# Performance work log

Hardware: AMD Instinct MI355X
Metric: run time of the kernel (lower is better)

The kernel has to match this reference:

```python
import jax, jax.numpy as jnp
import numpy as np

D_MODEL = 1024
N_BLOCK = 20
EPS = 1e-8


def setup_inputs() -> dict:
    key = jax.random.key(0)
    k = jax.random.split(key, 7)
    B, S, D, NB = 8, 2048, D_MODEL, N_BLOCK
    e = jax.random.normal(k[0], (B, S, D), dtype=jnp.float32)
    m = jax.random.normal(k[1], (B, S, D), dtype=jnp.float32)
    state = jax.random.normal(k[2], (1, NB * D), dtype=jnp.float32)
    # learned params of the EntNet-style RNN_cell
    U = jax.random.normal(k[3], (D, D), dtype=jnp.float32) * 0.02
    V = jax.random.normal(k[4], (D, D), dtype=jnp.float32) * 0.02
    W = jax.random.normal(k[5], (D, D), dtype=jnp.float32) * 0.02
    keys = jax.random.normal(k[6], (NB, D), dtype=jnp.float32) * 0.02
    return {"e": e, "m": m, "state": state, "U": U, "V": V, "W": W, "keys": keys}


def reference(e, m, state, U, V, W, keys):
    B, S, D = e.shape
    NB = keys.shape[0]
    h0 = state.reshape(NB, D)  # shared initial memory state across batch
    x = e + m  # combined per-timestep input, (B, S, D)

    def step(h, xt):  # h: (NB, D), xt: (D,)
        # per-slot gate: content similarity + key similarity
        g = jax.nn.sigmoid(h @ xt + keys @ xt)  # (NB,)
        # candidate memory
        cand = jnp.tanh(h @ U.T + keys @ V.T + (W @ xt)[None, :])  # (NB, D)
        h = h + g[:, None] * cand
        # per-slot L2 normalization
        h = h / (jnp.linalg.norm(h, axis=1, keepdims=True) + EPS)
        return h, None

    def run(xseq):  # xseq: (S, D) -> final state (NB, D)
        hT, _ = jax.lax.scan(step, h0, xseq)
        return hT

    out = jax.vmap(run)(x)  # (B, NB, D)
    return out
```

## Files before the change

### kernel.cpp

```cpp
#include <hip/hip_runtime.h>
#include <cstdint>
#include <cstddef>

namespace {

constexpr int D   = 1024;
constexpr int NB  = 20;
constexpr int B   = 8;
constexpr int S   = 2048;
constexpr int NWG = 32;
constexpr float EPS = 1e-8f;

typedef __attribute__((ext_vector_type(4))) float f4_t;
typedef __attribute__((ext_vector_type(8))) short s8_t;
typedef unsigned long long u64_t;

__device__ __forceinline__ unsigned short f2bf(float f) {
  unsigned u = __float_as_uint(f);
  u += 0x7fffu + ((u >> 16) & 1u);
  return (unsigned short)(u >> 16);
}
__device__ __forceinline__ float bf2f(unsigned short h) {
  return __uint_as_float(((unsigned)h) << 16);
}
__device__ __forceinline__ float u64lo(u64_t x) { return __uint_as_float((unsigned)x); }
__device__ __forceinline__ float u64hi(u64_t x) { return __uint_as_float((unsigned)(x >> 32)); }
__device__ __forceinline__ float rcp_f(float x) { return __builtin_amdgcn_rcpf(x); }
__device__ __forceinline__ float sigm_fast(float x) { return rcp_f(1.0f + __expf(-x)); }
__device__ __forceinline__ float tanh_fast(float x) {
  const float e = __expf(2.0f * x);
  return 1.0f - 2.0f * rcp_f(e + 1.0f);
}

#define MFMA(a, b, c) __builtin_amdgcn_mfma_f32_16x16x32_bf16((a), (b), (c), 0, 0, 0)
#define ALOAD64(p) __hip_atomic_load((p), __ATOMIC_RELAXED, __HIP_MEMORY_SCOPE_AGENT)
#define ASTORE64(p, v) __hip_atomic_store((p), (v), __ATOMIC_RELAXED, __HIP_MEMORY_SCOPE_AGENT)
#define ALOAD32(p) __hip_atomic_load((p), __ATOMIC_RELAXED, __HIP_MEMORY_SCOPE_AGENT)
#define ASTORE32(p, v) __hip_atomic_store((p), (v), __ATOMIC_RELAXED, __HIP_MEMORY_SCOPE_AGENT)

constexpr size_t OFF_HBUF = 0;
constexpr size_t OFF_NORM = OFF_HBUF + 2ull * B * NB * 512 * 4;
constexpr size_t OFF_CTR  = OFF_NORM + 2ull * B * NB * NWG * 4;
constexpr size_t OFF_KV   = OFF_CTR + (size_t)B * 32 * 4;
constexpr size_t OFF_KX   = OFF_KV + (size_t)NB * D * 4;
constexpr size_t OFF_UHI  = OFF_KX + (size_t)B * S * NB * 4;
constexpr size_t OFF_ULO  = OFF_UHI + (size_t)D * D * 2;
constexpr size_t OFF_WHI  = OFF_ULO + (size_t)D * D * 2;
constexpr size_t OFF_WLO  = OFF_WHI + (size_t)D * D * 2;


__global__ void k_convert(const float* __restrict__ U, const float* __restrict__ W,
                          unsigned short* __restrict__ Uhi, unsigned short* __restrict__ Ulo,
                          unsigned short* __restrict__ Whi, unsigned short* __restrict__ Wlo) {
  const int n = D * D;
  for (int i = blockIdx.x * blockDim.x + threadIdx.x; i < n; i += gridDim.x * blockDim.x) {
    float u = U[i];
    unsigned short h = f2bf(u);
    Uhi[i] = h;
    Ulo[i] = f2bf(u - bf2f(h));
    float w = W[i];
    h = f2bf(w);
    Whi[i] = h;
    Wlo[i] = f2bf(w - bf2f(h));
  }
}

__global__ void k_kv(const float* __restrict__ keys, const float* __restrict__ V,
                     float* __restrict__ KV) {
  const int tid = threadIdx.x;
  const int j = blockIdx.x * 64 + (tid >> 2);
  const int kq = tid & 3;
  const f4_t* v4 = (const f4_t*)(V + (size_t)j * D + kq * 256);
  const f4_t* k4base = (const f4_t*)keys;
  float acc[NB];
#pragma unroll
  for (int i = 0; i < NB; ++i) acc[i] = 0.f;
  for (int q = 0; q < 64; ++q) {
    const f4_t v = v4[q];
#pragma unroll
    for (int i = 0; i < NB; ++i) {
      const f4_t kk = k4base[i * 256 + kq * 64 + q];
      acc[i] += kk[0] * v[0] + kk[1] * v[1] + kk[2] * v[2] + kk[3] * v[3];
    }
  }
#pragma unroll
  for (int i = 0; i < NB; ++i) {
    float s = acc[i];
    s += __shfl_xor(s, 1);
    s += __shfl_xor(s, 2);
    if (kq == 0) KV[(size_t)i * D + j] = s;
  }
}

__global__ void k_kx(const float* __restrict__ e, const float* __restrict__ m,
                     const float* __restrict__ keys, float* __restrict__ KX) {
  __shared__ f4_t xs[256];
  __shared__ float part[NB][8];
  const int bt = blockIdx.x, tid = threadIdx.x;
  xs[tid] = ((const f4_t*)e)[(size_t)bt * 256 + tid] + ((const f4_t*)m)[(size_t)bt * 256 + tid];
  __syncthreads();
  if (tid < 160) {
    const int i = tid >> 3, s8 = tid & 7;
    float acc = 0.f;
    const f4_t* k4 = (const f4_t*)keys + i * 256 + s8 * 32;
    for (int q = 0; q < 32; ++q) {
      const f4_t kk = k4[q];
      const f4_t xx = xs[s8 * 32 + q];
      acc += kk[0] * xx[0] + kk[1] * xx[1] + kk[2] * xx[2] + kk[3] * xx[3];
    }
    part[i][s8] = acc;
  }
  __syncthreads();
  if (tid < NB) {
    float s = 0.f;
#pragma unroll
    for (int q = 0; q < 8; ++q) s += part[tid][q];
    KX[(size_t)bt * NB + tid] = s;
  }
}

__global__ void k_state(const float* __restrict__ state, unsigned* __restrict__ Hbuf,
                        float* __restrict__ NormP, int* __restrict__ ctr) {
  const int idx = blockIdx.x * 256 + threadIdx.x;
  if (idx < B * NB * 512) {
    const int r = idx % (NB * 512);
    const int i = r >> 9, d2 = (r & 511) << 1;
    const unsigned short a = f2bf(state[i * D + d2]);
    const unsigned short c = f2bf(state[i * D + d2 + 1]);
    Hbuf[idx] = (unsigned)a | ((unsigned)c << 16);
  }
  const int j = idx - B * NB * 512;
  if (j >= 0 && j < B * NB * NWG) NormP[j] = 1.0f / 32.0f;
  const int q = idx - B * NB * 512 - B * NB * NWG;
  if (q >= 0 && q < B * 32) ctr[q] = 0;
}


struct __align__(16) LdsT {
  unsigned short hnA[NB * 1024];
  unsigned short xtA[2][1024];
  float credU[4][2][2][16][20];
  float wxAcc[4][2][16];
  float gAcc[4][2][16];
  float KVs[NB][32];
  float ownH[NB][32];
  float pad_force_1_block_per_cu[3072];
};

__device__ __forceinline__ void build_xt(unsigned short* xt , int tid, f4_t x) {
  const unsigned short h0 = f2bf(x[0]), h1 = f2bf(x[1]), h2 = f2bf(x[2]), h3 = f2bf(x[3]);
  const unsigned short u0 = f2bf(x[0] - bf2f(h0)), u1 = f2bf(x[1] - bf2f(h1));
  const unsigned short u2 = f2bf(x[2] - bf2f(h2)), u3 = f2bf(x[3] - bf2f(h3));
  const int kp = tid << 2;
  *(unsigned*)&xt[kp] = (unsigned)h0 | ((unsigned)h1 << 16);
  *(unsigned*)&xt[kp + 2] = (unsigned)h2 | ((unsigned)h3 << 16);
  *(unsigned*)&xt[1024 + kp] = (unsigned)u0 | ((unsigned)u1 << 16);
  *(unsigned*)&xt[1024 + kp + 2] = (unsigned)u2 | ((unsigned)u3 << 16);
}

__device__ __forceinline__ void stage_h(unsigned short* hn, int tid, const u64_t* hv) {
  const int blkk = tid >> 1;
  const int half = (tid & 1) << 2;
#pragma unroll
  for (int j = 0; j < 20; ++j)
    *(u64_t*)&hn[(j << 10) + ((blkk ^ (j & 15)) << 3) + half] = hv[j];
}

__device__ __forceinline__ void bar_lds() {
  asm volatile("s_waitcnt lgkmcnt(0)\n\ts_barrier" ::: "memory");
}
__device__ __forceinline__ void bar_full() {
  asm volatile("s_waitcnt vmcnt(0) lgkmcnt(0)\n\ts_barrier" ::: "memory");
}

__device__ __forceinline__ void poll32(const unsigned* fb, int ln31, int wg,
                                       unsigned tgt, unsigned pv) {
  if (__ballot(pv >= tgt) == ~0ull) return;
  for (;;) {
    const unsigned v = (ln31 == wg) ? tgt : ALOAD32(fb + ln31);
    if (__ballot(v >= tgt) == ~0ull) return;
    __builtin_amdgcn_s_sleep(1);
  }
}

__launch_bounds__(256, 1)
__global__ void k_rnn(const float* __restrict__ e, const float* __restrict__ m,
                      const float* __restrict__ state,
                      const float* __restrict__ KX, const float* __restrict__ KV,
                      const unsigned short* __restrict__ Uhi, const unsigned short* __restrict__ Ulo,
                      const unsigned short* __restrict__ Whi, const unsigned short* __restrict__ Wlo,
                      unsigned* __restrict__ Hbuf, float* __restrict__ NormP,
                      int* __restrict__ ctr, float* __restrict__ out) {
  __shared__ LdsT L;
  const int tid = threadIdx.x;
  const int b = blockIdx.x >> 5;
  const int wg = blockIdx.x & 31;
  const int wv = tid >> 6;
  const int ln = tid & 63;
  const int l15 = ln & 15;
  const int lo4 = ln >> 4;
  const int ln31 = tid & 31;
  unsigned* ctrp = (unsigned*)ctr + b * 32;

  s8_t BUh[2][8], BUl[2][8], BWh[2][8], BWl[2][8];
  {
    const int rowb = (wg << 5) + l15;
#pragma unroll
    for (int nt = 0; nt < 2; ++nt)
#pragma unroll
      for (int kf = 0; kf < 8; ++kf) {
        const size_t off = (size_t)(rowb + nt * 16) * D + (wv << 8) + (kf << 5) + (lo4 << 3);
        BUh[nt][kf] = *(const s8_t*)(Uhi + off);
        BUl[nt][kf] = *(const s8_t*)(Ulo + off);
        BWh[nt][kf] = *(const s8_t*)(Whi + off);
        BWl[nt][kf] = *(const s8_t*)(Wlo + off);
      }
  }
  if (tid < 160) {
    const int i = tid >> 3, c4 = (tid & 7) << 2;
    *(f4_t*)&L.ownH[i][c4] = *(const f4_t*)(state + (size_t)i * D + (wg << 5) + c4);
    *(f4_t*)&L.KVs[i][c4] = *(const f4_t*)(KV + (size_t)i * D + (wg << 5) + c4);
  }

  f4_t evv, mvv;
  float sreg = 1.f;
  float kxreg = 0.f;

  {
    u64_t hv[20];
    const u64_t* hb8 = (const u64_t*)Hbuf + (size_t)(0 * B + b) * (NB * 256);
#pragma unroll
    for (int j = 0; j < 20; ++j) hv[j] = ALOAD64(hb8 + j * 256 + tid);
    const f4_t x0 = ((const f4_t*)e)[(size_t)(b * S) * 256 + tid] +
                    ((const f4_t*)m)[(size_t)(b * S) * 256 + tid];
    build_xt(&L.xtA[0][0], tid, x0);
    stage_h(L.hnA, tid, hv);
    if (tid < 160) kxreg = KX[(size_t)(b * S) * NB + (tid >> 3)];
    evv = ((const f4_t*)e)[(size_t)(b * S + 1) * 256 + tid];
    mvv = ((const f4_t*)m)[(size_t)(b * S + 1) * 256 + tid];
  }
  __syncthreads();

  for (int t = 0; t < S; ++t) {
    const int nxt2 = (t + 1) & 1;

    f4_t cU00 = {0, 0, 0, 0}, cU01 = {0, 0, 0, 0}, cU10 = {0, 0, 0, 0}, cU11 = {0, 0, 0, 0};
    f4_t cW0 = {0, 0, 0, 0}, cW1 = {0, 0, 0, 0}, cG0 = {0, 0, 0, 0}, cG1 = {0, 0, 0, 0};
    {
      const unsigned short* hb = L.hnA;
      const unsigned short* xb = &L.xtA[0][0];
      const int r1 = 16 + (l15 < 4 ? l15 : 3);
#pragma unroll
      for (int kf = 0; kf < 8; ++kf) {
        const int blk = (wv << 5) + (kf << 2) + lo4;
        const s8_t a0 = *(const s8_t*)&hb[(l15 << 10) + ((blk ^ l15) << 3)];
        const s8_t a1 = *(const s8_t*)&hb[(r1 << 10) + ((blk ^ (r1 & 15)) << 3)];
        const s8_t ax = *(const s8_t*)&xb[(l15 & 1) * 1024 + (blk << 3)];
        cU00 = MFMA(a0, BUh[0][kf], cU00);
        cU00 = MFMA(a0, BUl[0][kf], cU00);
        cU01 = MFMA(a0, BUh[1][kf], cU01);
        cU01 = MFMA(a0, BUl[1][kf], cU01);
        cU10 = MFMA(a1, BUh[0][kf], cU10);
        cU10 = MFMA(a1, BUl[0][kf], cU10);
        cU11 = MFMA(a1, BUh[1][kf], cU11);
        cU11 = MFMA(a1, BUl[1][kf], cU11);
        cW0 = MFMA(ax, BWh[0][kf], cW0);
        cW0 = MFMA(ax, BWl[0][kf], cW0);
        cW1 = MFMA(ax, BWh[1][kf], cW1);
        cW1 = MFMA(ax, BWl[1][kf], cW1);
        cG0 = MFMA(ax, a0, cG0);
        cG1 = MFMA(ax, a1, cG1);
      }
    }
#pragma unroll
    for (int q = 0; q < 4; ++q) {
      const int r = (lo4 << 2) + q;
      L.credU[wv][0][0][r][l15] = cU00[q];
      L.credU[wv][0][1][r][l15] = cU01[q];
      L.credU[wv][1][0][r][l15] = cU10[q];
      L.credU[wv][1][1][r][l15] = cU11[q];
    }
    if (lo4 == 0) {
      L.wxAcc[wv][0][l15] = cW0[0] + cW0[1];
      L.wxAcc[wv][1][l15] = cW1[0] + cW1[1];
      L.gAcc[wv][0][l15] = cG0[0] + cG0[1];
      L.gAcc[wv][1][l15] = cG1[0] + cG1[1];
    }
    bar_lds();

    unsigned pv = 0;
    if (t + 1 < S) pv = (ln31 == wg) ? (unsigned)(t + 1) : ALOAD32(ctrp + ln31);

    if (tid < 160) {
      const int i = tid >> 3, c4 = (tid & 7) << 2;
      const int mt = i >> 4, r = i & 15, nt = c4 >> 4, ccc = c4 & 15;
      const f4_t sU = *(const f4_t*)&L.credU[0][mt][nt][r][ccc] +
                      *(const f4_t*)&L.credU[1][mt][nt][r][ccc] +
                      *(const f4_t*)&L.credU[2][mt][nt][r][ccc] +
                      *(const f4_t*)&L.credU[3][mt][nt][r][ccc];
      const f4_t wx = *(const f4_t*)&L.wxAcc[0][nt][ccc] +
                      *(const f4_t*)&L.wxAcc[1][nt][ccc] +
                      *(const f4_t*)&L.wxAcc[2][nt][ccc] +
                      *(const f4_t*)&L.wxAcc[3][nt][ccc];
      const f4_t kv = *(const f4_t*)&L.KVs[i][c4];
      const f4_t oh = *(const f4_t*)&L.ownH[i][c4];
      const float s = sreg;
      const float gpre = s * (L.gAcc[0][mt][r] + L.gAcc[1][mt][r] +
                              L.gAcc[2][mt][r] + L.gAcc[3][mt][r]) + kxreg;
      const float g = sigm_fast(gpre);
      f4_t hn;
      float sq = 0.f;
#pragma unroll
      for (int u = 0; u < 4; ++u) {
        const float cand = tanh_fast(s * sU[u] + kv[u] + wx[u]);
        const float hx = s * oh[u] + g * cand;
        hn[u] = hx;
        sq += hx * hx;
      }
      *(f4_t*)&L.ownH[i][c4] = hn;
      const unsigned d0 = (unsigned)f2bf(hn[0]) | ((unsigned)f2bf(hn[1]) << 16);
      const unsigned d1 = (unsigned)f2bf(hn[2]) | ((unsigned)f2bf(hn[3]) << 16);
      u64_t* hb8 = (u64_t*)Hbuf + (size_t)(nxt2 * B + b) * (NB * 256) +
                   (i << 8) + (wg << 3) + (c4 >> 2);
      ASTORE64(hb8, (u64_t)d0 | ((u64_t)d1 << 32));
      sq += __shfl_xor(sq, 1);
      sq += __shfl_xor(sq, 2);
      sq += __shfl_xor(sq, 4);
      if ((tid & 7) == 0) {
        unsigned* np = (unsigned*)NormP + ((size_t)(nxt2 * B + b) * NB + i) * NWG + wg;
        ASTORE32(np, __float_as_uint(sq));
      }
    }
    bar_full();

    if (tid == 0) ASTORE32(ctrp + wg, (unsigned)(t + 1));

    if (t + 1 < S) {
      poll32(ctrp, ln31, wg, (unsigned)(t + 1), pv);
      u64_t hv[20];
      const u64_t* g0 = (const u64_t*)Hbuf + (size_t)(nxt2 * B + b) * (NB * 256);
#pragma unroll
      for (int j = 0; j < 20; ++j) hv[j] = ALOAD64(g0 + j * 256 + tid);
      float np0 = 0.f;
      if (tid < 160) {
        const int i = tid >> 3;
        const u64_t* n0 = (const u64_t*)NormP + ((size_t)(nxt2 * B + b) * NB + i) * 16 + ((tid & 7) << 1);
        const u64_t a0 = ALOAD64(n0);
        const u64_t a1 = ALOAD64(n0 + 1);
        np0 = u64lo(a0) + u64hi(a0) + u64lo(a1) + u64hi(a1);
        kxreg = KX[((size_t)b * S + t + 1) * NB + i];
      }
      build_xt(&L.xtA[0][0], tid, evv + mvv);
      if (t + 2 < S) {
        evv = ((const f4_t*)e)[(size_t)(b * S + t + 2) * 256 + tid];
        mvv = ((const f4_t*)m)[(size_t)(b * S + t + 2) * 256 + tid];
      }
      stage_h(L.hnA, tid, hv);
      if (tid < 160) {
        float s0 = np0;
        s0 += __shfl_xor(s0, 1);
        s0 += __shfl_xor(s0, 2);
        s0 += __shfl_xor(s0, 4);
        sreg = rcp_f(sqrtf(s0) + EPS);
      }
    }
    bar_lds();
  }

  poll32(ctrp, ln31, wg, (unsigned)S, 0u);
  if (tid < 160) {
    const int i = tid >> 3, c4 = (tid & 7) << 2;
    const u64_t* np8 = (const u64_t*)NormP + ((size_t)(0 * B + b) * NB + i) * 16 + ((tid & 7) << 1);
    const u64_t x0 = ALOAD64(np8);
    const u64_t x1 = ALOAD64(np8 + 1);
    float sq = u64lo(x0) + u64hi(x0) + u64lo(x1) + u64hi(x1);
    sq += __shfl_xor(sq, 1);
    sq += __shfl_xor(sq, 2);
    sq += __shfl_xor(sq, 4);
    const float sc = rcp_f(sqrtf(sq) + EPS);
    const f4_t oh = *(const f4_t*)&L.ownH[i][c4];
    f4_t ov;
#pragma unroll
    for (int u = 0; u < 4; ++u) ov[u] = sc * oh[u];
    *(f4_t*)(out + (size_t)b * NB * D + (size_t)i * D + (wg << 5) + c4) = ov;
  }
}

}

extern "C" void kernel_launch(void* const* d_in, const int* in_sizes, int n_in,
                              void* d_out, int out_size, void* d_ws, size_t ws_size,
                              hipStream_t stream) {
  const float* e = (const float*)d_in[0];
  const float* m = (const float*)d_in[1];
  const float* state = (const float*)d_in[2];
  const float* U = (const float*)d_in[3];
  const float* V = (const float*)d_in[4];
  const float* W = (const float*)d_in[5];
  const float* keys = (const float*)d_in[6];
  float* out = (float*)d_out;
  char* ws = (char*)d_ws;

  unsigned* Hbuf = (unsigned*)(ws + OFF_HBUF);
  float* NormP = (float*)(ws + OFF_NORM);
  int* ctr = (int*)(ws + OFF_CTR);
  float* KV = (float*)(ws + OFF_KV);
  float* KX = (float*)(ws + OFF_KX);
  unsigned short* Uhi = (unsigned short*)(ws + OFF_UHI);
  unsigned short* Ulo = (unsigned short*)(ws + OFF_ULO);
  unsigned short* Whi = (unsigned short*)(ws + OFF_WHI);
  unsigned short* Wlo = (unsigned short*)(ws + OFF_WLO);

  k_convert<<<512, 256, 0, stream>>>(U, W, Uhi, Ulo, Whi, Wlo);
  k_kv<<<16, 256, 0, stream>>>(keys, V, KV);
  k_kx<<<B * S, 256, 0, stream>>>(e, m, keys, KX);
  k_state<<<342, 256, 0, stream>>>(state, Hbuf, NormP, ctr);
  k_rnn<<<B * NWG, 256, 0, stream>>>(e, m, state, KX, KV, Uhi, Ulo, Whi, Wlo,
                                     Hbuf, NormP, ctr, out);
}
```

Before: 11.89 ms.

## Double workgroup size to 512 threads splitting K across 8 waves

```diff
diff --git a/kernel.cpp b/kernel.cpp
--- a/kernel.cpp
+++ b/kernel.cpp
@@ -11,6 +11,7 @@
 constexpr int NWG = 32;
 constexpr float EPS = 1e-8f;
 
+typedef __attribute__((ext_vector_type(2))) float f2_t;
 typedef __attribute__((ext_vector_type(4))) float f4_t;
 typedef __attribute__((ext_vector_type(8))) short s8_t;
 typedef unsigned long long u64_t;
@@ -139,31 +140,30 @@
 struct __align__(16) LdsT {
   unsigned short hnA[NB * 1024];
   unsigned short xtA[2][1024];
-  float credU[4][2][2][16][20];
-  float wxAcc[4][2][16];
-  float gAcc[4][2][16];
+  float credU[8][2][2][16][20];
+  float wxAcc[8][2][16];
+  float gAcc[8][2][16];
   float KVs[NB][32];
   float ownH[NB][32];
-  float pad_force_1_block_per_cu[3072];
 };
 
-__device__ __forceinline__ void build_xt(unsigned short* xt , int tid, f4_t x) {
-  const unsigned short h0 = f2bf(x[0]), h1 = f2bf(x[1]), h2 = f2bf(x[2]), h3 = f2bf(x[3]);
+__device__ __forceinline__ void build_xt(unsigned short* xt , int tid, f2_t x) {
+  const unsigned short h0 = f2bf(x[0]), h1 = f2bf(x[1]);
   const unsigned short u0 = f2bf(x[0] - bf2f(h0)), u1 = f2bf(x[1] - bf2f(h1));
-  const unsigned short u2 = f2bf(x[2] - bf2f(h2)), u3 = f2bf(x[3] - bf2f(h3));
-  const int kp = tid << 2;
+  const int kp = tid << 1;
   *(unsigned*)&xt[kp] = (unsigned)h0 | ((unsigned)h1 << 16);
-  *(unsigned*)&xt[kp + 2] = (unsigned)h2 | ((unsigned)h3 << 16);
   *(unsigned*)&xt[1024 + kp] = (unsigned)u0 | ((unsigned)u1 << 16);
-  *(unsigned*)&xt[1024 + kp + 2] = (unsigned)u2 | ((unsigned)u3 << 16);
-}
-
-__device__ __forceinline__ void stage_h(unsigned short* hn, int tid, const u64_t* hv) {
-  const int blkk = tid >> 1;
-  const int half = (tid & 1) << 2;
-#pragma unroll
-  for (int j = 0; j < 20; ++j)
-    *(u64_t*)&hn[(j << 10) + ((blkk ^ (j & 15)) << 3) + half] = hv[j];
+}
+
+__device__ __forceinline__ void stage_h(unsigned short* hn, int t8, int rbase,
+                                        const u64_t* hv) {
+  const int blkk = t8 >> 1;
+  const int halfo = (t8 & 1) << 2;
+#pragma unroll
+  for (int j = 0; j < 10; ++j) {
+    const int jr = rbase + j;
+    *(u64_t*)&hn[(jr << 10) + ((blkk ^ (jr & 15)) << 3) + halfo] = hv[j];
+  }
 }
 
 __device__ __forceinline__ void bar_lds() {
@@ -183,7 +183,7 @@
   }
 }
 
-__launch_bounds__(256, 1)
+__launch_bounds__(512, 2)
 __global__ void k_rnn(const float* __restrict__ e, const float* __restrict__ m,
                       const float* __restrict__ state,
                       const float* __restrict__ KX, const float* __restrict__ KV,
@@ -193,23 +193,25 @@
                       int* __restrict__ ctr, float* __restrict__ out) {
   __shared__ LdsT L;
   const int tid = threadIdx.x;
-  const int b = blockIdx.x >> 5;
-  const int wg = blockIdx.x & 31;
+  const int b = blockIdx.x & 7;
+  const int wg = blockIdx.x >> 3;
   const int wv = tid >> 6;
   const int ln = tid & 63;
   const int l15 = ln & 15;
   const int lo4 = ln >> 4;
   const int ln31 = tid & 31;
+  const int t8 = tid & 255;
+  const int rbase = (tid >> 8) * 10;
   unsigned* ctrp = (unsigned*)ctr + b * 32;
 
-  s8_t BUh[2][8], BUl[2][8], BWh[2][8], BWl[2][8];
+  s8_t BUh[2][4], BUl[2][4], BWh[2][4], BWl[2][4];
   {
     const int rowb = (wg << 5) + l15;
 #pragma unroll
     for (int nt = 0; nt < 2; ++nt)
 #pragma unroll
-      for (int kf = 0; kf < 8; ++kf) {
-        const size_t off = (size_t)(rowb + nt * 16) * D + (wv << 8) + (kf << 5) + (lo4 << 3);
+      for (int kf = 0; kf < 4; ++kf) {
+        const size_t off = (size_t)(rowb + nt * 16) * D + (wv << 7) + (kf << 5) + (lo4 << 3);
         BUh[nt][kf] = *(const s8_t*)(Uhi + off);
         BUl[nt][kf] = *(const s8_t*)(Ulo + off);
         BWh[nt][kf] = *(const s8_t*)(Whi + off);
@@ -222,22 +224,22 @@
     *(f4_t*)&L.KVs[i][c4] = *(const f4_t*)(KV + (size_t)i * D + (wg << 5) + c4);
   }
 
-  f4_t evv, mvv;
+  f2_t evv, mvv;
   float sreg = 1.f;
   float kxreg = 0.f;
 
   {
-    u64_t hv[20];
+    u64_t hv[10];
     const u64_t* hb8 = (const u64_t*)Hbuf + (size_t)(0 * B + b) * (NB * 256);
 #pragma unroll
-    for (int j = 0; j < 20; ++j) hv[j] = ALOAD64(hb8 + j * 256 + tid);
-    const f4_t x0 = ((const f4_t*)e)[(size_t)(b * S) * 256 + tid] +
-                    ((const f4_t*)m)[(size_t)(b * S) * 256 + tid];
+    for (int j = 0; j < 10; ++j) hv[j] = ALOAD64(hb8 + (rbase + j) * 256 + t8);
+    const f2_t x0 = ((const f2_t*)e)[(size_t)(b * S) * 512 + tid] +
+                    ((const f2_t*)m)[(size_t)(b * S) * 512 + tid];
     build_xt(&L.xtA[0][0], tid, x0);
-    stage_h(L.hnA, tid, hv);
+    stage_h(L.hnA, t8, rbase, hv);
     if (tid < 160) kxreg = KX[(size_t)(b * S) * NB + (tid >> 3)];
-    evv = ((const f4_t*)e)[(size_t)(b * S + 1) * 256 + tid];
-    mvv = ((const f4_t*)m)[(size_t)(b * S + 1) * 256 + tid];
+    evv = ((const f2_t*)e)[(size_t)(b * S + 1) * 512 + tid];
+    mvv = ((const f2_t*)m)[(size_t)(b * S + 1) * 512 + tid];
   }
   __syncthreads();
 
@@ -251,8 +253,8 @@
       const unsigned short* xb = &L.xtA[0][0];
       const int r1 = 16 + (l15 < 4 ? l15 : 3);
 #pragma unroll
-      for (int kf = 0; kf < 8; ++kf) {
-        const int blk = (wv << 5) + (kf << 2) + lo4;
+      for (int kf = 0; kf < 4; ++kf) {
+        const int blk = (wv << 4) + (kf << 2) + lo4;
         const s8_t a0 = *(const s8_t*)&hb[(l15 << 10) + ((blk ^ l15) << 3)];
         const s8_t a1 = *(const s8_t*)&hb[(r1 << 10) + ((blk ^ (r1 & 15)) << 3)];
         const s8_t ax = *(const s8_t*)&xb[(l15 & 1) * 1024 + (blk << 3)];
@@ -294,20 +296,18 @@
     if (tid < 160) {
       const int i = tid >> 3, c4 = (tid & 7) << 2;
       const int mt = i >> 4, r = i & 15, nt = c4 >> 4, ccc = c4 & 15;
-      const f4_t sU = *(const f4_t*)&L.credU[0][mt][nt][r][ccc] +
-                      *(const f4_t*)&L.credU[1][mt][nt][r][ccc] +
-                      *(const f4_t*)&L.credU[2][mt][nt][r][ccc] +
-                      *(const f4_t*)&L.credU[3][mt][nt][r][ccc];
-      const f4_t wx = *(const f4_t*)&L.wxAcc[0][nt][ccc] +
-                      *(const f4_t*)&L.wxAcc[1][nt][ccc] +
-                      *(const f4_t*)&L.wxAcc[2][nt][ccc] +
-                      *(const f4_t*)&L.wxAcc[3][nt][ccc];
+      f4_t sU = {0, 0, 0, 0}, wx = {0, 0, 0, 0};
+      float gp = 0.f;
+#pragma unroll
+      for (int w = 0; w < 8; ++w) {
+        sU += *(const f4_t*)&L.credU[w][mt][nt][r][ccc];
+        wx += *(const f4_t*)&L.wxAcc[w][nt][ccc];
+        gp += L.gAcc[w][mt][r];
+      }
       const f4_t kv = *(const f4_t*)&L.KVs[i][c4];
       const f4_t oh = *(const f4_t*)&L.ownH[i][c4];
       const float s = sreg;
-      const float gpre = s * (L.gAcc[0][mt][r] + L.gAcc[1][mt][r] +
-                              L.gAcc[2][mt][r] + L.gAcc[3][mt][r]) + kxreg;
-      const float g = sigm_fast(gpre);
+      const float g = sigm_fast(s * gp + kxreg);
       f4_t hn;
       float sq = 0.f;
 #pragma unroll
@@ -337,10 +337,10 @@
 
     if (t + 1 < S) {
       poll32(ctrp, ln31, wg, (unsigned)(t + 1), pv);
-      u64_t hv[20];
+      u64_t hv[10];
       const u64_t* g0 = (const u64_t*)Hbuf + (size_t)(nxt2 * B + b) * (NB * 256);
 #pragma unroll
-      for (int j = 0; j < 20; ++j) hv[j] = ALOAD64(g0 + j * 256 + tid);
+      for (int j = 0; j < 10; ++j) hv[j] = ALOAD64(g0 + (rbase + j) * 256 + t8);
       float np0 = 0.f;
       if (tid < 160) {
         const int i = tid >> 3;
@@ -352,10 +352,10 @@
       }
       build_xt(&L.xtA[0][0], tid, evv + mvv);
       if (t + 2 < S) {
-        evv = ((const f4_t*)e)[(size_t)(b * S + t + 2) * 256 + tid];
-        mvv = ((const f4_t*)m)[(size_t)(b * S + t + 2) * 256 + tid];
-      }
-      stage_h(L.hnA, tid, hv);
+        evv = ((const f2_t*)e)[(size_t)(b * S + t + 2) * 512 + tid];
+        mvv = ((const f2_t*)m)[(size_t)(b * S + t + 2) * 512 + tid];
+      }
+      stage_h(L.hnA, t8, rbase, hv);
       if (tid < 160) {
         float s0 = np0;
         s0 += __shfl_xor(s0, 1);
@@ -415,6 +415,6 @@
   k_kv<<<16, 256, 0, stream>>>(keys, V, KV);
   k_kx<<<B * S, 256, 0, stream>>>(e, m, keys, KX);
   k_state<<<342, 256, 0, stream>>>(state, Hbuf, NormP, ctr);
-  k_rnn<<<B * NWG, 256, 0, stream>>>(e, m, state, KX, KV, Uhi, Ulo, Whi, Wlo,
+  k_rnn<<<B * NWG, 512, 0, stream>>>(e, m, state, KX, KV, Uhi, Ulo, Whi, Wlo,
                                      Hbuf, NormP, ctr, out);
 }
```

Measured after the change: 16.70 ms. 40.5% more time.

## Replace workgroup barrier with per-wave flags in cross-WG step synchronization

Applied to the files above, without the earlier changes.

```diff
diff --git a/kernel.cpp b/kernel.cpp
--- a/kernel.cpp
+++ b/kernel.cpp
@@ -41,7 +41,7 @@
 constexpr size_t OFF_HBUF = 0;
 constexpr size_t OFF_NORM = OFF_HBUF + 2ull * B * NB * 512 * 4;
 constexpr size_t OFF_CTR  = OFF_NORM + 2ull * B * NB * NWG * 4;
-constexpr size_t OFF_KV   = OFF_CTR + (size_t)B * 32 * 4;
+constexpr size_t OFF_KV   = OFF_CTR + (size_t)B * 32 * 4 * 4;
 constexpr size_t OFF_KX   = OFF_KV + (size_t)NB * D * 4;
 constexpr size_t OFF_UHI  = OFF_KX + (size_t)B * S * NB * 4;
 constexpr size_t OFF_ULO  = OFF_UHI + (size_t)D * D * 2;
@@ -132,7 +132,7 @@
   const int j = idx - B * NB * 512;
   if (j >= 0 && j < B * NB * NWG) NormP[j] = 1.0f / 32.0f;
   const int q = idx - B * NB * 512 - B * NB * NWG;
-  if (q >= 0 && q < B * 32) ctr[q] = 0;
+  if (q >= 0 && q < B * 32 * 4) ctr[q] = 0;
 }
 
 
@@ -169,18 +169,19 @@
 __device__ __forceinline__ void bar_lds() {
   asm volatile("s_waitcnt lgkmcnt(0)\n\ts_barrier" ::: "memory");
 }
-__device__ __forceinline__ void bar_full() {
-  asm volatile("s_waitcnt vmcnt(0) lgkmcnt(0)\n\ts_barrier" ::: "memory");
-}
-
-__device__ __forceinline__ void poll32(const unsigned* fb, int ln31, int wg,
-                                       unsigned tgt, unsigned pv) {
-  if (__ballot(pv >= tgt) == ~0ull) return;
+
+__device__ __forceinline__ void poll96(const unsigned* fb, int ln31, unsigned tgt) {
+  const unsigned* p = fb + (ln31 << 2);
   for (;;) {
-    const unsigned v = (ln31 == wg) ? tgt : ALOAD32(fb + ln31);
-    if (__ballot(v >= tgt) == ~0ull) return;
+    const unsigned v0 = ALOAD32(p);
+    const unsigned v1 = ALOAD32(p + 1);
+    const unsigned v2 = ALOAD32(p + 2);
+    unsigned mn = v0 < v1 ? v0 : v1;
+    mn = mn < v2 ? mn : v2;
+    if (__ballot(mn >= tgt) == ~0ull) break;
     __builtin_amdgcn_s_sleep(1);
   }
+  asm volatile("" ::: "memory");
 }
 
 __launch_bounds__(256, 1)
@@ -193,14 +194,14 @@
                       int* __restrict__ ctr, float* __restrict__ out) {
   __shared__ LdsT L;
   const int tid = threadIdx.x;
-  const int b = blockIdx.x >> 5;
-  const int wg = blockIdx.x & 31;
+  const int b = blockIdx.x & 7;
+  const int wg = blockIdx.x >> 3;
   const int wv = tid >> 6;
   const int ln = tid & 63;
   const int l15 = ln & 15;
   const int lo4 = ln >> 4;
   const int ln31 = tid & 31;
-  unsigned* ctrp = (unsigned*)ctr + b * 32;
+  unsigned* ctrp = (unsigned*)ctr + b * 128;
 
   s8_t BUh[2][8], BUl[2][8], BWh[2][8], BWl[2][8];
   {
@@ -288,8 +289,7 @@
     }
     bar_lds();
 
-    unsigned pv = 0;
-    if (t + 1 < S) pv = (ln31 == wg) ? (unsigned)(t + 1) : ALOAD32(ctrp + ln31);
+    if (t + 1 < S) build_xt(&L.xtA[0][0], tid, evv + mvv);
 
     if (tid < 160) {
       const int i = tid >> 3, c4 = (tid & 7) << 2;
@@ -331,12 +331,14 @@
         ASTORE32(np, __float_as_uint(sq));
       }
     }
-    bar_full();
-
-    if (tid == 0) ASTORE32(ctrp + wg, (unsigned)(t + 1));
+
+    if (wv < 3) {
+      asm volatile("s_waitcnt vmcnt(0)" ::: "memory");
+      if (ln == 0) ASTORE32(ctrp + (wg << 2) + wv, (unsigned)(t + 1));
+    }
 
     if (t + 1 < S) {
-      poll32(ctrp, ln31, wg, (unsigned)(t + 1), pv);
+      poll96(ctrp, ln31, (unsigned)(t + 1));
       u64_t hv[20];
       const u64_t* g0 = (const u64_t*)Hbuf + (size_t)(nxt2 * B + b) * (NB * 256);
 #pragma unroll
@@ -350,11 +352,6 @@
         np0 = u64lo(a0) + u64hi(a0) + u64lo(a1) + u64hi(a1);
         kxreg = KX[((size_t)b * S + t + 1) * NB + i];
       }
-      build_xt(&L.xtA[0][0], tid, evv + mvv);
-      if (t + 2 < S) {
-        evv = ((const f4_t*)e)[(size_t)(b * S + t + 2) * 256 + tid];
-        mvv = ((const f4_t*)m)[(size_t)(b * S + t + 2) * 256 + tid];
-      }
       stage_h(L.hnA, tid, hv);
       if (tid < 160) {
         float s0 = np0;
@@ -363,11 +360,15 @@
         s0 += __shfl_xor(s0, 4);
         sreg = rcp_f(sqrtf(s0) + EPS);
       }
-    }
-    bar_lds();
-  }
-
-  poll32(ctrp, ln31, wg, (unsigned)S, 0u);
+      if (t + 2 < S) {
+        evv = ((const f4_t*)e)[(size_t)(b * S + t + 2) * 256 + tid];
+        mvv = ((const f4_t*)m)[(size_t)(b * S + t + 2) * 256 + tid];
+      }
+      asm volatile("s_waitcnt lgkmcnt(0)" ::: "memory");
+    }
+  }
+
+  poll96(ctrp, ln31, (unsigned)S);
   if (tid < 160) {
     const int i = tid >> 3, c4 = (tid & 7) << 2;
     const u64_t* np8 = (const u64_t*)NormP + ((size_t)(0 * B + b) * NB + i) * 16 + ((tid & 7) << 1);
@@ -414,7 +415,7 @@
   k_convert<<<512, 256, 0, stream>>>(U, W, Uhi, Ulo, Whi, Wlo);
   k_kv<<<16, 256, 0, stream>>>(keys, V, KV);
   k_kx<<<B * S, 256, 0, stream>>>(e, m, keys, KX);
-  k_state<<<342, 256, 0, stream>>>(state, Hbuf, NormP, ctr);
+  k_state<<<344, 256, 0, stream>>>(state, Hbuf, NormP, ctr);
   k_rnn<<<B * NWG, 256, 0, stream>>>(e, m, state, KX, KV, Uhi, Ulo, Whi, Wlo,
                                      Hbuf, NormP, ctr, out);
 }
```

After: 22.59 ms. 90.1% more time.
